# Optimization experiments

Measured on AMD Instinct MI355X. Metric: run time of the kernel, lower is better.

## Reference

```python
import jax, jax.numpy as jnp
import numpy as np

BATCH, IN_SIZE, CH, DIM, MODES, LAYERS, PROJ, OUT = 16, 1, 128, 128, 32, 4, 128, 1


def setup_inputs() -> dict:
    key = jax.random.key(0)
    ks = jax.random.split(key, 12)
    scale = 1.0 / (CH * CH)
    inp = {
        "z": jax.random.normal(ks[0], (BATCH, IN_SIZE, DIM, DIM), dtype=jnp.float32),
        # Lifting: pointwise linear input_size -> channels
        "lift_w": jax.random.normal(ks[1], (CH, IN_SIZE), dtype=jnp.float32) / np.sqrt(IN_SIZE),
        "lift_b": jnp.zeros((CH,), dtype=jnp.float32),
        # Spectral conv weights per layer, two mode corners, complex stored as real/imag
        "wr1": scale * jax.random.normal(ks[2], (LAYERS, CH, CH, MODES, MODES), dtype=jnp.float32),
        "wi1": scale * jax.random.normal(ks[3], (LAYERS, CH, CH, MODES, MODES), dtype=jnp.float32),
        "wr2": scale * jax.random.normal(ks[4], (LAYERS, CH, CH, MODES, MODES), dtype=jnp.float32),
        "wi2": scale * jax.random.normal(ks[5], (LAYERS, CH, CH, MODES, MODES), dtype=jnp.float32),
        # Projection: channels -> projection_size -> output_size (pointwise MLP)
        "pw1": jax.random.normal(ks[6], (PROJ, CH), dtype=jnp.float32) / np.sqrt(CH),
        "pb1": jnp.zeros((PROJ,), dtype=jnp.float32),
        "pw2": jax.random.normal(ks[7], (OUT, PROJ), dtype=jnp.float32) / np.sqrt(PROJ),
        "pb2": jnp.zeros((OUT,), dtype=jnp.float32),
    }
    return inp


def _spectral_conv(v, w1, w2, modes, size):
    # v: [b, c, X, Y] real; rfft2 over last two dims (norm='backward')
    vf = jnp.fft.rfft2(v, norm="backward")  # [b, c, X, Y//2+1] complex
    of = jnp.zeros_like(vf)
    # low-frequency corner
    of = of.at[:, :, :modes, :modes].set(
        jnp.einsum("bixy,ioxy->boxy", vf[:, :, :modes, :modes], w1))
    # high (negative) frequency corner along first spatial axis
    of = of.at[:, :, -modes:, :modes].set(
        jnp.einsum("bixy,ioxy->boxy", vf[:, :, -modes:, :modes], w2))
    return jnp.fft.irfft2(of, s=(size, size), norm="backward")


def reference(z, lift_w, lift_b, wr1, wi1, wr2, wi2, pw1, pb1, pw2, pb2):
    n_layers = wr1.shape[0]
    modes = wr1.shape[-1]
    size = z.shape[-1]
    # Lifting: [b, in, x, y] -> [b, ch, x, y]
    v = jnp.einsum("bixy,ci->bcxy", z, lift_w) + lift_b[None, :, None, None]
    out = v
    for l in range(n_layers):
        w1 = wr1[l] + 1j * wi1[l]
        w2 = wr2[l] + 1j * wi2[l]
        out = _spectral_conv(out, w1, w2, modes, size)
    # Projection MLP (pointwise over grid)
    h = jnp.einsum("bcxy,pc->bpxy", out, pw1) + pb1[None, :, None, None]
    h = jax.nn.gelu(h)
    out = jnp.einsum("bpxy,op->boxy", h, pw2) + pb2[None, :, None, None]
    return out
```

## Files before the change

kernel.cpp:

```cpp
#include <hip/hip_runtime.h>
#include <math.h>

#define B 16
#define CH 128
#define DIM 128
#define MODES 32
#define NLAYERS 4
#define PROJ 128
#define U 64
#define KY 32
#define NMODE (U*KY)
#define N2 (DIM*DIM)
#define PG 32
#define PPG (PROJ/PG)

__device__ __forceinline__ void async16(const void* g, void* l) {
  __builtin_amdgcn_global_load_lds((const __attribute__((address_space(1))) unsigned int*)g,
                                   (__attribute__((address_space(3))) unsigned int*)l, 16, 0, 0);
}

__global__ __launch_bounds__(256) void k_zf1(const float* __restrict__ z,
                                             float2* __restrict__ t1) {
  __shared__ float zrow[16][DIM];
  __shared__ float2 tw[DIM];
  int bid = blockIdx.x;
  int b = bid >> 3, xt = bid & 7;
  int x0 = xt * 16;
  int t = threadIdx.x;
  if (t < 128) {
    float ang = (float)(2.0 * M_PI) * (float)t / 128.0f;
    tw[t] = make_float2(cosf(ang), sinf(ang));
  }
  for (int e = t; e < 16 * DIM / 4; e += 256)
    ((float4*)&zrow[0][0])[e] = ((const float4*)&z[b * N2 + x0 * DIM])[e];
  __syncthreads();
  #pragma unroll
  for (int j = 0; j < 2; ++j) {
    int it = t + j * 256;
    int x_l = it >> 5, ky = it & 31;
    float tr = 0.f, ti = 0.f;
    for (int y = 0; y < DIM; ++y) {
      float v = zrow[x_l][y];
      float2 w = tw[(ky * y) & 127];
      tr += v * w.x;
      ti -= v * w.y;
    }
    t1[((size_t)b * DIM + x0 + x_l) * KY + ky] = make_float2(tr, ti);
  }
}

__global__ __launch_bounds__(256) void k_zf2(const float2* __restrict__ t1,
                                             float* __restrict__ zfr, float* __restrict__ zfi) {
  __shared__ float2 t1s[DIM][KY];
  __shared__ float2 tw[DIM];
  int bid = blockIdx.x;
  int b = bid >> 1, uh = bid & 1;
  int t = threadIdx.x;
  if (t < 128) {
    float ang = (float)(2.0 * M_PI) * (float)t / 128.0f;
    tw[t] = make_float2(cosf(ang), sinf(ang));
  }
  for (int e = t; e < DIM * KY / 2; e += 256)
    ((float4*)&t1s[0][0])[e] = ((const float4*)&t1[(size_t)b * DIM * KY])[e];
  __syncthreads();
  #pragma unroll
  for (int j = 0; j < 4; ++j) {
    int m = t + j * 256;
    int u_l = m >> 5, ky = m & 31;
    int u = uh * 32 + u_l;
    int kx = (u < 32) ? u : (u + 64);
    float ar = 0.f, ai = 0.f;
    for (int x = 0; x < DIM; ++x) {
      float2 v = t1s[x][ky];
      float2 w = tw[(kx * x) & 127];
      ar += v.x * w.x + v.y * w.y;
      ai += v.y * w.x - v.x * w.y;
    }
    zfr[b * NMODE + u * KY + ky] = ar;
    zfi[b * NMODE + u * KY + ky] = ai;
  }
}

__global__ __launch_bounds__(256) void k_lift(const float* __restrict__ zfr, const float* __restrict__ zfi,
                                              const float* __restrict__ lw, const float* __restrict__ lb,
                                              float2* __restrict__ vcout) {
  int idx = blockIdx.x * 256 + threadIdx.x;
  if (idx >= B * CH * NMODE) return;
  int m = idx & (NMODE - 1);
  int c = (idx >> 11) & 127;
  int b = idx >> 18;
  float w = lw[c];
  float re = w * zfr[b * NMODE + m];
  float im = w * zfi[b * NMODE + m];
  if (m == 0) re += 16384.f * lb[c];
  vcout[idx] = make_float2(re, im);
}

__global__ __launch_bounds__(256) void k_spec(const float2* __restrict__ vc,
                                              const float* __restrict__ wr1, const float* __restrict__ wi1,
                                              const float* __restrict__ wr2, const float* __restrict__ wi2,
                                              float2* __restrict__ oc) {
  __shared__ float lW[2][2][4][16][32];
  __shared__ float2 lV[2][4][16][32];
  int bid = blockIdx.x;
  int u = ((bid & 7) << 3) | ((bid >> 3) & 7);
  int ot = bid >> 6;
  int o0 = ot * 16;
  int kxw = u & 31;
  const float* wr = (u >= 32) ? wr2 : wr1;
  const float* wi = (u >= 32) ? wi2 : wi1;
  int t = threadIdx.x;
  int ky = t & 31, bh = (t >> 5) & 1, oq = t >> 6;
  int wv = t >> 6, lane = t & 63;
  float accR[4][8] = {}, accI[4][8] = {};

  #define STAGE(bf, i0)                                                              \
    {                                                                                \
      if (wv < 2) {                                                                  \
        _Pragma("unroll")                                                            \
        for (int n = 0; n < 8; ++n) {                                                \
          int nu = wv * 8 + n;                                                       \
          int ri = nu >> 3, il = (nu >> 1) & 3;                                      \
          int o_l = (nu & 1) * 8 + (lane >> 3), ky4 = (lane & 7) * 4;                \
          const float* src = (ri ? wi : wr) +                                        \
            (((size_t)((i0) + il) * CH + o0 + o_l) * MODES + kxw) * MODES + ky4;     \
          async16(src, (char*)&lW[bf][0][0][0][0] + (size_t)nu * 1024 + lane * 16);  \
        }                                                                            \
      } else {                                                                       \
        _Pragma("unroll")                                                            \
        for (int n = 0; n < 8; ++n) {                                                \
          int nu = (wv - 2) * 8 + n;                                                 \
          int il = nu >> 2;                                                          \
          int b_l = (nu & 3) * 4 + (lane >> 4), ky2 = (lane & 15) * 2;               \
          const float2* src = vc + ((size_t)b_l * CH + (i0) + il) * NMODE +          \
                              u * KY + ky2;                                          \
          async16(src, (char*)&lV[bf][0][0][0] + (size_t)nu * 1024 + lane * 16);     \
        }                                                                            \
      }                                                                              \
    }

  STAGE(0, 0);
  for (int k = 0; k < 32; ++k) {
    int cur = k & 1;
    __syncthreads();
    if (k + 1 < 32) STAGE(cur ^ 1, (k + 1) * 4);
    #pragma unroll
    for (int il = 0; il < 4; ++il) {
      float wrv[4], wiv[4];
      #pragma unroll
      for (int j = 0; j < 4; ++j) {
        wrv[j] = lW[cur][0][il][oq * 4 + j][ky];
        wiv[j] = lW[cur][1][il][oq * 4 + j][ky];
      }
      #pragma unroll
      for (int bb = 0; bb < 8; ++bb) {
        float2 v = lV[cur][il][bh * 8 + bb][ky];
        #pragma unroll
        for (int j = 0; j < 4; ++j) {
          accR[j][bb] += wrv[j] * v.x - wiv[j] * v.y;
          accI[j][bb] += wrv[j] * v.y + wiv[j] * v.x;
        }
      }
    }
  }
  #undef STAGE
  #pragma unroll
  for (int j = 0; j < 4; ++j)
    #pragma unroll
    for (int bb = 0; bb < 8; ++bb) {
      int o = o0 + oq * 4 + j, b = bh * 8 + bb;
      oc[(((size_t)b * CH + o) * U + u) * KY + ky] = make_float2(accR[j][bb], accI[j][bb]);
    }
}

__global__ __launch_bounds__(256) void k_proj0(float2* __restrict__ vc) {
  int idx = blockIdx.x * 256 + threadIdx.x;
  if (idx >= B * CH * 33) return;
  int pi = idx % 33;
  int bc = idx / 33;
  float2* base = vc + (size_t)bc * NMODE;
  if (pi == 0) {
    base[0].y = 0.f;
  } else if (pi == 32) {
    base[32 * KY].x *= 0.5f;
    base[32 * KY].y *= 0.5f;
  } else {
    int ua = pi, ub = 64 - pi;
    float2 a = base[ua * KY], b2 = base[ub * KY];
    base[ua * KY] = make_float2(0.5f * (a.x + b2.x), 0.5f * (a.y - b2.y));
    base[ub * KY] = make_float2(0.5f * (b2.x + a.x), 0.5f * (b2.y - a.y));
  }
}

__global__ __launch_bounds__(256) void k_pw1(const float2* __restrict__ xc,
                                             const float* __restrict__ pw1,
                                             float2* __restrict__ hc) {
  __shared__ float wT[CH][CH + 1];
  int bid = blockIdx.x;
  int b = ((bid & 7) << 1) | ((bid >> 8) & 1);
  int jt = (bid >> 3) & 31;
  int t = threadIdx.x;
  for (int e = t; e < CH * CH; e += 256) {
    int p = e >> 7, c = e & 127;
    wT[c][p] = pw1[e];
  }
  __syncthreads();
  int tx = t & 15, ty = t >> 4;
  int j0 = jt * 64 + tx * 4;
  float accR[4][8] = {}, accI[4][8] = {};
  for (int c = 0; c < CH; ++c) {
    const float4* x4 = (const float4*)&xc[((size_t)b * CH + c) * NMODE + j0];
    float4 v0 = x4[0], v1 = x4[1];
    float xrv[4] = {v0.x, v0.z, v1.x, v1.z};
    float xiv[4] = {v0.y, v0.w, v1.y, v1.w};
    float w[8];
    #pragma unroll
    for (int pp = 0; pp < 8; ++pp) w[pp] = wT[c][ty * 8 + pp];
    #pragma unroll
    for (int jj = 0; jj < 4; ++jj)
      #pragma unroll
      for (int pp = 0; pp < 8; ++pp) {
        accR[jj][pp] += w[pp] * xrv[jj];
        accI[jj][pp] += w[pp] * xiv[jj];
      }
  }
  #pragma unroll
  for (int pp = 0; pp < 8; ++pp) {
    int p = ty * 8 + pp;
    float4* o4 = (float4*)&hc[((size_t)b * CH + p) * NMODE + j0];
    o4[0] = make_float4(accR[0][pp], accI[0][pp], accR[1][pp], accI[1][pp]);
    o4[1] = make_float4(accR[2][pp], accI[2][pp], accR[3][pp], accI[3][pp]);
  }
}

__global__ __launch_bounds__(256) void k_idft_partial(const float2* __restrict__ hc,
                                                      const float* __restrict__ pb1,
                                                      const float* __restrict__ pw2,
                                                      float* __restrict__ partial) {
  __shared__ float2 tw[DIM];
  __shared__ float2 hfs[2][NMODE];
  __shared__ float2 sbuf[16][KY];
  int bid = blockIdx.x;
  int b = (bid & 7) | (((bid >> 3) & 1) << 3);
  int pg = (bid >> 4) & 31, xs = bid >> 9;
  int x0 = xs * 8;
  int t = threadIdx.x;
  int wv = t >> 6, lane = t & 63;
  if (t < 128) {
    float ang = (float)(2.0 * M_PI) * (float)t / 128.0f;
    tw[t] = make_float2(cosf(ang), sinf(ang));
  }

  #define STAGE_H(bf, pp_)                                                           \
    {                                                                                \
      const char* srcb = (const char*)(hc + ((size_t)b * CH + pg * PPG + (pp_)) * NMODE); \
      _Pragma("unroll")                                                              \
      for (int n = 0; n < 4; ++n) {                                                  \
        int nu = wv * 4 + n;                                                         \
        async16(srcb + (size_t)nu * 1024 + lane * 16,                                \
                (char*)&hfs[bf][0] + (size_t)nu * 1024 + lane * 16);                 \
      }                                                                              \
    }

  STAGE_H(0, 0);
  __syncthreads();
  int y = t & 63, xh = t >> 6;
  float Cr[KY], Sr[KY];
  #pragma unroll
  for (int ky = 0; ky < KY; ++ky) {
    float2 w = tw[(ky * y) & 127];
    float wk = (ky == 0) ? 1.f : 2.f;
    Cr[ky] = wk * w.x;
    Sr[ky] = -wk * w.y;
  }
  int xqA = t >> 5, kyA = t & 31;
  int xA = x0 + xqA;
  float res[8] = {0.f, 0.f, 0.f, 0.f, 0.f, 0.f, 0.f, 0.f};
  for (int pp = 0; pp < PPG; ++pp) {
    int p = pg * PPG + pp;
    int cur = pp & 1;
    if (pp) __syncthreads();
    if (pp + 1 < PPG) STAGE_H(cur ^ 1, pp + 1);
    {
      float per = 0.f, pei = 0.f, por = 0.f, poi = 0.f;
      #pragma unroll
      for (int uu = 0; uu < 32; uu += 2) {
        float2 w0 = tw[(uu * xA) & 127];
        float2 h0 = hfs[cur][uu * KY + kyA];
        per += h0.x * w0.x - h0.y * w0.y;
        pei += h0.x * w0.y + h0.y * w0.x;
        float2 w1 = tw[((uu + 1) * xA) & 127];
        float2 h1 = hfs[cur][(uu + 1) * KY + kyA];
        por += h1.x * w1.x - h1.y * w1.y;
        poi += h1.x * w1.y + h1.y * w1.x;
      }
      #pragma unroll
      for (int uu = 32; uu < 64; uu += 2) {
        float2 w0 = tw[((uu + 64) * xA) & 127];
        float2 h0 = hfs[cur][uu * KY + kyA];
        per += h0.x * w0.x - h0.y * w0.y;
        pei += h0.x * w0.y + h0.y * w0.x;
        float2 w1 = tw[((uu + 65) * xA) & 127];
        float2 h1 = hfs[cur][(uu + 1) * KY + kyA];
        por += h1.x * w1.x - h1.y * w1.y;
        poi += h1.x * w1.y + h1.y * w1.x;
      }
      sbuf[xqA][kyA]     = make_float2(per + por, pei + poi);
      sbuf[xqA + 8][kyA] = make_float2(per - por, pei - poi);
    }
    __syncthreads();
    float pb = pb1[p], pw = pw2[p];
    #pragma unroll
    for (int sl = 0; sl < 4; ++sl) {
      int s_i = xh + sl * 4;
      float ae = 0.f, ao = 0.f;
      #pragma unroll
      for (int ky = 0; ky < KY; ky += 2) {
        float4 v = *(const float4*)&sbuf[s_i][ky];
        ae += v.x * Cr[ky] + v.y * Sr[ky];
        ao += v.z * Cr[ky + 1] + v.w * Sr[ky + 1];
      }
      float hlo = (ae + ao) * (1.f / 16384.f) + pb;
      float hhi = (ae - ao) * (1.f / 16384.f) + pb;
      float zlo = 1.5957691216057308f * (hlo + 0.044715f * hlo * hlo * hlo);
      float zhi = 1.5957691216057308f * (hhi + 0.044715f * hhi * hhi * hhi);
      res[sl * 2]     += pw * hlo * __builtin_amdgcn_rcpf(1.f + __expf(-zlo));
      res[sl * 2 + 1] += pw * hhi * __builtin_amdgcn_rcpf(1.f + __expf(-zhi));
    }
  }
  #undef STAGE_H
  size_t pbase = ((size_t)pg * B + b) * N2;
  #pragma unroll
  for (int sl = 0; sl < 4; ++sl) {
    int s_i = xh + sl * 4;
    int x = x0 + (s_i & 7) + ((s_i >> 3) << 6);
    partial[pbase + x * DIM + y]      = res[sl * 2];
    partial[pbase + x * DIM + y + 64] = res[sl * 2 + 1];
  }
}

__global__ __launch_bounds__(256) void k_reduce(const float* __restrict__ partial,
                                                const float* __restrict__ pb2,
                                                float* __restrict__ outp) {
  int idx = blockIdx.x * 256 + threadIdx.x;
  if (idx >= B * N2) return;
  float s = pb2[0];
  #pragma unroll
  for (int pg = 0; pg < PG; ++pg) s += partial[(size_t)pg * B * N2 + idx];
  outp[idx] = s;
}

extern "C" void kernel_launch(void* const* d_in, const int* in_sizes, int n_in,
                              void* d_out, int out_size, void* d_ws, size_t ws_size,
                              hipStream_t stream) {
  const float* z   = (const float*)d_in[0];
  const float* lw  = (const float*)d_in[1];
  const float* lb  = (const float*)d_in[2];
  const float* wr1 = (const float*)d_in[3];
  const float* wi1 = (const float*)d_in[4];
  const float* wr2 = (const float*)d_in[5];
  const float* wi2 = (const float*)d_in[6];
  const float* pw1 = (const float*)d_in[7];
  const float* pb1 = (const float*)d_in[8];
  const float* pw2 = (const float*)d_in[9];
  const float* pb2 = (const float*)d_in[10];
  float* out = (float*)d_out;
  float* ws = (float*)d_ws;

  float* zfr = ws;
  float* zfi = zfr + 32768;
  float2* Ac = (float2*)(ws + 65536);
  float2* Bc = Ac + (size_t)B * CH * NMODE;
  float2* t1 = Bc;

  k_zf1<<<B * 8, 256, 0, stream>>>(z, t1);
  k_zf2<<<B * 2, 256, 0, stream>>>(t1, zfr, zfi);
  k_lift<<<(B * CH * NMODE) / 256, 256, 0, stream>>>(zfr, zfi, lw, lb, Ac);

  const size_t WSTRIDE = (size_t)CH * CH * MODES * MODES;
  float2 *ir = Ac, *oc = Bc;
  for (int l = 0; l < NLAYERS; ++l) {
    k_spec<<<512, 256, 0, stream>>>(ir,
                                    wr1 + l * WSTRIDE, wi1 + l * WSTRIDE,
                                    wr2 + l * WSTRIDE, wi2 + l * WSTRIDE,
                                    oc);
    if (l < NLAYERS - 1)
      k_proj0<<<(B * CH * 33 + 255) / 256, 256, 0, stream>>>(oc);
    float2* tmp = ir; ir = oc; oc = tmp;
  }
  k_pw1<<<512, 256, 0, stream>>>(ir, pw1, oc);
  float* partial = (float*)ir;
  k_idft_partial<<<B * PG * 8, 256, 0, stream>>>(oc, pb1, pw2, partial);
  k_reduce<<<(B * N2) / 256, 256, 0, stream>>>(partial, pb2, out);
}
```

Baseline: 793.0 us.

## Deepen spectral-conv prefetch and enlarge inverse-DFT tiles with twiddle recurrence

The spectral mode-mixing kernel now keeps two weight/activation stages in flight. It waits with explicit vmcnt counts and raw barriers, where before it prefetched one stage and called __syncthreads. The inverse-DFT projection kernel gives each block 32 x-rows instead of 8 and launches a quarter as many blocks, so the per-block setup and staged hc loads are amortised over more output. Its row stage now uses vectorised LDS reads and a complex-multiply twiddle recurrence. The risks are higher register pressure from the 32 accumulators, fewer blocks for occupancy, and small drift from the recurrence's rounding.

```diff
diff --git a/kernel.cpp b/kernel.cpp
--- a/kernel.cpp
+++ b/kernel.cpp
@@ -140,10 +140,17 @@
     }
 
   STAGE(0, 0);
+  STAGE(1, 4);
   for (int k = 0; k < 32; ++k) {
     int cur = k & 1;
-    __syncthreads();
-    if (k + 1 < 32) STAGE(cur ^ 1, (k + 1) * 4);
+    if (k < 31) {
+      asm volatile("s_waitcnt vmcnt(8)" ::: "memory");
+    } else {
+      asm volatile("s_waitcnt vmcnt(0)" ::: "memory");
+    }
+    __builtin_amdgcn_s_barrier();
+    asm volatile("" ::: "memory");
+    __builtin_amdgcn_sched_barrier(0);
     #pragma unroll
     for (int il = 0; il < 4; ++il) {
       float wrv[4], wiv[4];
@@ -162,6 +169,9 @@
         }
       }
     }
+    __builtin_amdgcn_s_barrier();
+    asm volatile("" ::: "memory");
+    if (k + 2 < 32) STAGE(cur, (k + 2) * 4);
   }
   #undef STAGE
   #pragma unroll
@@ -239,11 +249,11 @@
                                                       float* __restrict__ partial) {
   __shared__ float2 tw[DIM];
   __shared__ float2 hfs[2][NMODE];
-  __shared__ float2 sbuf[16][KY];
+  __shared__ float2 sbuf[64][KY + 2];
   int bid = blockIdx.x;
   int b = (bid & 7) | (((bid >> 3) & 1) << 3);
   int pg = (bid >> 4) & 31, xs = bid >> 9;
-  int x0 = xs * 8;
+  int x0 = xs * 32;
   int t = threadIdx.x;
   int wv = t >> 6, lane = t & 63;
   if (t < 128) {
@@ -273,46 +283,66 @@
     Cr[ky] = wk * w.x;
     Sr[ky] = -wk * w.y;
   }
-  int xqA = t >> 5, kyA = t & 31;
+  int xqA = t >> 3;
+  int ky0 = (t & 7) * 4;
   int xA = x0 + xqA;
-  float res[8] = {0.f, 0.f, 0.f, 0.f, 0.f, 0.f, 0.f, 0.f};
+  float2 r2 = tw[(2 * xA) & 127];
+  float res[32];
+  #pragma unroll
+  for (int i = 0; i < 32; ++i) res[i] = 0.f;
+
   for (int pp = 0; pp < PPG; ++pp) {
     int p = pg * PPG + pp;
     int cur = pp & 1;
-    if (pp) __syncthreads();
+    if (pp) {
+      asm volatile("s_waitcnt vmcnt(0)" ::: "memory");
+      __builtin_amdgcn_s_barrier();
+      asm volatile("" ::: "memory");
+    }
     if (pp + 1 < PPG) STAGE_H(cur ^ 1, pp + 1);
     {
-      float per = 0.f, pei = 0.f, por = 0.f, poi = 0.f;
-      #pragma unroll
-      for (int uu = 0; uu < 32; uu += 2) {
-        float2 w0 = tw[(uu * xA) & 127];
-        float2 h0 = hfs[cur][uu * KY + kyA];
-        per += h0.x * w0.x - h0.y * w0.y;
-        pei += h0.x * w0.y + h0.y * w0.x;
-        float2 w1 = tw[((uu + 1) * xA) & 127];
-        float2 h1 = hfs[cur][(uu + 1) * KY + kyA];
-        por += h1.x * w1.x - h1.y * w1.y;
-        poi += h1.x * w1.y + h1.y * w1.x;
-      }
-      #pragma unroll
-      for (int uu = 32; uu < 64; uu += 2) {
-        float2 w0 = tw[((uu + 64) * xA) & 127];
-        float2 h0 = hfs[cur][uu * KY + kyA];
-        per += h0.x * w0.x - h0.y * w0.y;
-        pei += h0.x * w0.y + h0.y * w0.x;
-        float2 w1 = tw[((uu + 65) * xA) & 127];
-        float2 h1 = hfs[cur][(uu + 1) * KY + kyA];
-        por += h1.x * w1.x - h1.y * w1.y;
-        poi += h1.x * w1.y + h1.y * w1.x;
-      }
-      sbuf[xqA][kyA]     = make_float2(per + por, pei + poi);
-      sbuf[xqA + 8][kyA] = make_float2(per - por, pei - poi);
-    }
-    __syncthreads();
+      float per[4] = {}, pei[4] = {}, por[4] = {}, poi[4] = {};
+      float2 we = make_float2(1.f, 0.f), wo = tw[xA & 127];
+      #pragma unroll
+      for (int half = 0; half < 2; ++half) {
+        #pragma unroll
+        for (int pr = 0; pr < 16; ++pr) {
+          int uu = half * 32 + pr * 2;
+          if ((pr & 3) == 0) {
+            int kxe = half * 96 + pr * 2;
+            we = tw[(kxe * xA) & 127];
+            wo = tw[((kxe + 1) * xA) & 127];
+          }
+          float4 e01 = *(const float4*)&hfs[cur][uu * KY + ky0];
+          float4 e23 = *(const float4*)&hfs[cur][uu * KY + ky0 + 2];
+          float4 o01 = *(const float4*)&hfs[cur][(uu + 1) * KY + ky0];
+          float4 o23 = *(const float4*)&hfs[cur][(uu + 1) * KY + ky0 + 2];
+          per[0] += e01.x * we.x - e01.y * we.y;  pei[0] += e01.x * we.y + e01.y * we.x;
+          per[1] += e01.z * we.x - e01.w * we.y;  pei[1] += e01.z * we.y + e01.w * we.x;
+          per[2] += e23.x * we.x - e23.y * we.y;  pei[2] += e23.x * we.y + e23.y * we.x;
+          per[3] += e23.z * we.x - e23.w * we.y;  pei[3] += e23.z * we.y + e23.w * we.x;
+          por[0] += o01.x * wo.x - o01.y * wo.y;  poi[0] += o01.x * wo.y + o01.y * wo.x;
+          por[1] += o01.z * wo.x - o01.w * wo.y;  poi[1] += o01.z * wo.y + o01.w * wo.x;
+          por[2] += o23.x * wo.x - o23.y * wo.y;  poi[2] += o23.x * wo.y + o23.y * wo.x;
+          por[3] += o23.z * wo.x - o23.w * wo.y;  poi[3] += o23.z * wo.y + o23.w * wo.x;
+          float2 wen = make_float2(we.x * r2.x - we.y * r2.y, we.x * r2.y + we.y * r2.x);
+          float2 won = make_float2(wo.x * r2.x - wo.y * r2.y, wo.x * r2.y + wo.y * r2.x);
+          we = wen; wo = won;
+        }
+      }
+      #pragma unroll
+      for (int q = 0; q < 4; ++q) {
+        sbuf[xqA][ky0 + q]      = make_float2(per[q] + por[q], pei[q] + poi[q]);
+        sbuf[xqA + 32][ky0 + q] = make_float2(per[q] - por[q], pei[q] - poi[q]);
+      }
+    }
+    asm volatile("s_waitcnt lgkmcnt(0)" ::: "memory");
+    __builtin_amdgcn_s_barrier();
+    asm volatile("" ::: "memory");
     float pb = pb1[p], pw = pw2[p];
     #pragma unroll
-    for (int sl = 0; sl < 4; ++sl) {
-      int s_i = xh + sl * 4;
+    for (int sl = 0; sl < 16; ++sl) {
+      int s_i = xh * 16 + sl;
       float ae = 0.f, ao = 0.f;
       #pragma unroll
       for (int ky = 0; ky < KY; ky += 2) {
@@ -327,13 +357,17 @@
       res[sl * 2]     += pw * hlo * __builtin_amdgcn_rcpf(1.f + __expf(-zlo));
       res[sl * 2 + 1] += pw * hhi * __builtin_amdgcn_rcpf(1.f + __expf(-zhi));
     }
+    if (pp + 1 < PPG) {
+      __builtin_amdgcn_s_barrier();
+      asm volatile("" ::: "memory");
+    }
   }
   #undef STAGE_H
   size_t pbase = ((size_t)pg * B + b) * N2;
   #pragma unroll
-  for (int sl = 0; sl < 4; ++sl) {
-    int s_i = xh + sl * 4;
-    int x = x0 + (s_i & 7) + ((s_i >> 3) << 6);
+  for (int sl = 0; sl < 16; ++sl) {
+    int s_i = xh * 16 + sl;
+    int x = x0 + (s_i & 31) + ((s_i >> 5) << 6);
     partial[pbase + x * DIM + y]      = res[sl * 2];
     partial[pbase + x * DIM + y + 64] = res[sl * 2 + 1];
   }
@@ -390,6 +424,6 @@
   }
   k_pw1<<<512, 256, 0, stream>>>(ir, pw1, oc);
   float* partial = (float*)ir;
-  k_idft_partial<<<B * PG * 8, 256, 0, stream>>>(oc, pb1, pw2, partial);
+  k_idft_partial<<<B * PG * 2, 256, 0, stream>>>(oc, pb1, pw2, partial);
   k_reduce<<<(B * N2) / 256, 256, 0, stream>>>(partial, pb2, out);
 }
```

New measurement: 2.055 ms. 159% more time.

## Load spectral weights directly into registers instead of staging through LDS

Applied to the files above, without the earlier changes.

The spectral mixing kernel no longer stages weight tiles in shared memory. Each thread now reads its own weight values straight from global memory into registers, double-buffered across two register sets, while only the activation tile keeps going through async LDS loads. This cuts LDS traffic and LDS footprint, and launch bounds now ask for two blocks per CU. In exchange it uses more registers, and the per-thread weight loads are strided and only partly coalesced (32 consecutive ky per row).

```diff
diff --git a/kernel.cpp b/kernel.cpp
--- a/kernel.cpp
+++ b/kernel.cpp
@@ -96,11 +96,10 @@
   vcout[idx] = make_float2(re, im);
 }
 
-__global__ __launch_bounds__(256) void k_spec(const float2* __restrict__ vc,
-                                              const float* __restrict__ wr1, const float* __restrict__ wi1,
-                                              const float* __restrict__ wr2, const float* __restrict__ wi2,
-                                              float2* __restrict__ oc) {
-  __shared__ float lW[2][2][4][16][32];
+__global__ __launch_bounds__(256, 2) void k_spec(const float2* __restrict__ vc,
+                                                 const float* __restrict__ wr1, const float* __restrict__ wi1,
+                                                 const float* __restrict__ wr2, const float* __restrict__ wi2,
+                                                 float2* __restrict__ oc) {
   __shared__ float2 lV[2][4][16][32];
   int bid = blockIdx.x;
   int u = ((bid & 7) << 3) | ((bid >> 3) & 7);
@@ -110,65 +109,77 @@
   const float* wr = (u >= 32) ? wr2 : wr1;
   const float* wi = (u >= 32) ? wi2 : wi1;
   int t = threadIdx.x;
-  int ky = t & 31, bh = (t >> 5) & 1, oq = t >> 6;
-  int wv = t >> 6, lane = t & 63;
+  int ky = t & 31, bh = (t >> 5) & 1, wv = t >> 6;
+  int lane = t & 63;
   float accR[4][8] = {}, accI[4][8] = {};
-
-  #define STAGE(bf, i0)                                                              \
+  const size_t wbase = ((size_t)(o0 + wv * 4) * MODES + kxw) * MODES + ky;
+
+  float wAr[4][4], wAi[4][4], wBr[4][4], wBi[4][4];
+
+  #define LOADW(R, I, c)                                                             \
     {                                                                                \
-      if (wv < 2) {                                                                  \
+      const float* pr = wr + wbase + (size_t)(c) * 4 * CH * 1024;                    \
+      const float* pi_ = wi + wbase + (size_t)(c) * 4 * CH * 1024;                   \
+      _Pragma("unroll")                                                              \
+      for (int il = 0; il < 4; ++il)                                                 \
         _Pragma("unroll")                                                            \
-        for (int n = 0; n < 8; ++n) {                                                \
-          int nu = wv * 8 + n;                                                       \
-          int ri = nu >> 3, il = (nu >> 1) & 3;                                      \
-          int o_l = (nu & 1) * 8 + (lane >> 3), ky4 = (lane & 7) * 4;                \
-          const float* src = (ri ? wi : wr) +                                        \
-            (((size_t)((i0) + il) * CH + o0 + o_l) * MODES + kxw) * MODES + ky4;     \
-          async16(src, (char*)&lW[bf][0][0][0][0] + (size_t)nu * 1024 + lane * 16);  \
+        for (int j = 0; j < 4; ++j) {                                                \
+          R[il][j] = pr[(size_t)(il * CH + j) * 1024];                               \
+          I[il][j] = pi_[(size_t)(il * CH + j) * 1024];                              \
         }                                                                            \
-      } else {                                                                       \
+    }
+
+  #define STAGEV(bf, c)                                                              \
+    {                                                                                \
+      _Pragma("unroll")                                                              \
+      for (int n = 0; n < 4; ++n) {                                                  \
+        int nu = wv * 4 + n;                                                         \
+        int row = nu * 4 + (lane >> 4);                                              \
+        int il = row >> 4, bl = row & 15;                                            \
+        const float2* src = vc + ((size_t)bl * CH + (c) * 4 + il) * NMODE +          \
+                            u * KY + (lane & 15) * 2;                                \
+        async16(src, (char*)&lV[bf][0][0][0] + (size_t)nu * 1024 + lane * 16);       \
+      }                                                                              \
+    }
+
+  #define COMPUTE(bf, R, I)                                                          \
+    {                                                                                \
+      _Pragma("unroll")                                                              \
+      for (int il = 0; il < 4; ++il)                                                 \
         _Pragma("unroll")                                                            \
-        for (int n = 0; n < 8; ++n) {                                                \
-          int nu = (wv - 2) * 8 + n;                                                 \
-          int il = nu >> 2;                                                          \
-          int b_l = (nu & 3) * 4 + (lane >> 4), ky2 = (lane & 15) * 2;               \
-          const float2* src = vc + ((size_t)b_l * CH + (i0) + il) * NMODE +          \
-                              u * KY + ky2;                                          \
-          async16(src, (char*)&lV[bf][0][0][0] + (size_t)nu * 1024 + lane * 16);     \
+        for (int bb = 0; bb < 8; ++bb) {                                             \
+          float2 v = lV[bf][il][bh * 8 + bb][ky];                                    \
+          _Pragma("unroll")                                                          \
+          for (int j = 0; j < 4; ++j) {                                              \
+            accR[j][bb] += R[il][j] * v.x - I[il][j] * v.y;                          \
+            accI[j][bb] += R[il][j] * v.y + I[il][j] * v.x;                          \
+          }                                                                          \
         }                                                                            \
-      }                                                                              \
-    }
-
-  STAGE(0, 0);
-  for (int k = 0; k < 32; ++k) {
-    int cur = k & 1;
+    }
+
+  LOADW(wAr, wAi, 0);
+  STAGEV(0, 0);
+  for (int k2 = 0; k2 < 16; ++k2) {
+    int c0 = k2 * 2;
     __syncthreads();
-    if (k + 1 < 32) STAGE(cur ^ 1, (k + 1) * 4);
-    #pragma unroll
-    for (int il = 0; il < 4; ++il) {
-      float wrv[4], wiv[4];
-      #pragma unroll
-      for (int j = 0; j < 4; ++j) {
-        wrv[j] = lW[cur][0][il][oq * 4 + j][ky];
-        wiv[j] = lW[cur][1][il][oq * 4 + j][ky];
-      }
-      #pragma unroll
-      for (int bb = 0; bb < 8; ++bb) {
-        float2 v = lV[cur][il][bh * 8 + bb][ky];
-        #pragma unroll
-        for (int j = 0; j < 4; ++j) {
-          accR[j][bb] += wrv[j] * v.x - wiv[j] * v.y;
-          accI[j][bb] += wrv[j] * v.y + wiv[j] * v.x;
-        }
-      }
-    }
-  }
-  #undef STAGE
+    STAGEV(1, c0 + 1);
+    LOADW(wBr, wBi, c0 + 1);
+    COMPUTE(0, wAr, wAi);
+    __syncthreads();
+    if (c0 + 2 < 32) {
+      STAGEV(0, c0 + 2);
+      LOADW(wAr, wAi, c0 + 2);
+    }
+    COMPUTE(1, wBr, wBi);
+  }
+  #undef LOADW
+  #undef STAGEV
+  #undef COMPUTE
   #pragma unroll
   for (int j = 0; j < 4; ++j)
     #pragma unroll
     for (int bb = 0; bb < 8; ++bb) {
-      int o = o0 + oq * 4 + j, b = bh * 8 + bb;
+      int o = o0 + wv * 4 + j, b = bh * 8 + bb;
       oc[(((size_t)b * CH + o) * U + u) * KY + ky] = make_float2(accR[j][bb], accI[j][bb]);
     }
 }
```

After: 919.1 us. 15.9% more time.
